# Kernel optimization log

Measured on AMD Instinct MI355X. Metric: run time of the kernel, lower is better.

## Reference

```python
import jax, jax.numpy as jnp
import numpy as np

B, S_IMG, S_TXT, S_BOK = 1, 2048, 512, 4
DM, H, DH, R = 3072, 24, 128, 16
LORA_SCALE, LORA_ALPHA, BOKEH_SCALE = 1.0, 16.0, 1.0
EPS = 1e-6


def _rms_norm(x, w):
    # normalize over head_dim (last axis), Flux RMSNorm eps=1e-6
    var = jnp.mean(jnp.square(x), axis=-1, keepdims=True)
    return x * jax.lax.rsqrt(var + EPS) * w


def _lora(x, w_down, w_up):
    # LoRALinear: up(down(x)) * alpha/rank
    return (x @ w_down.T) @ w_up.T * (LORA_ALPHA / R)


def _apply_rope(x, cos, sin):
    # x: [B,H,S,D]; cos/sin: [S,D]; diffusers use_real=True, unbind_dim=-1 (interleaved pairs)
    x1 = x[..., 0::2]
    x2 = x[..., 1::2]
    rot = jnp.stack([-x2, x1], axis=-1).reshape(x.shape)
    return x * cos[None, None] + rot * sin[None, None]


def _sdpa(q, k, v):
    # q:[B,H,Sq,D] k,v:[B,H,Sk,D]
    scale = 1.0 / jnp.sqrt(jnp.asarray(q.shape[-1], q.dtype))
    scores = jnp.einsum('bhqd,bhkd->bhqk', q, k) * scale
    p = jax.nn.softmax(scores, axis=-1)
    return jnp.einsum('bhqk,bhkd->bhqd', p, v)


def setup_inputs() -> dict:
    key = jax.random.key(0)
    ks = jax.random.split(key, 40)
    std = 0.02
    d = {}
    d['hidden_states'] = jax.random.normal(ks[0], (B, S_IMG, DM), jnp.float32)
    d['encoder_hidden_states'] = jax.random.normal(ks[1], (B, S_TXT, DM), jnp.float32)
    d['bokeh_embeds'] = jax.random.normal(ks[2], (B, S_BOK, DM), jnp.float32)
    theta = jax.random.uniform(ks[3], (S_TXT + S_IMG, DH // 2), jnp.float32) * 2 * np.pi
    theta = jnp.repeat(theta, 2, axis=-1)  # interleaved pairs share angle
    d['rope_cos'] = jnp.cos(theta)
    d['rope_sin'] = jnp.sin(theta)
    # base attention params
    for i, nm in enumerate(['Wq', 'Wk', 'Wv', 'Waq', 'Wak', 'Wav', 'Wo', 'Wao']):
        d[nm] = jax.random.normal(ks[4 + i], (DM, DM), jnp.float32) * std
    for i, nm in enumerate(['bq', 'bk', 'bv', 'baq', 'bak', 'bav', 'bo', 'bao']):
        d[nm] = jax.random.normal(ks[12 + i], (DM,), jnp.float32) * std
    for i, nm in enumerate(['norm_q_w', 'norm_k_w', 'norm_aq_w', 'norm_ak_w']):
        d[nm] = 1.0 + jax.random.normal(ks[20 + i], (DH,), jnp.float32) * std
    # LoRA adapters (up weights random, not zero, for nontrivial math)
    for i, nm in enumerate(['kb_down', 'vb_down', 'qadp_down', 'kadp_down']):
        d[nm] = jax.random.normal(ks[24 + i], (R, DM), jnp.float32) * (1.0 / R)
    for i, nm in enumerate(['kb_up', 'vb_up', 'qadp_up', 'kadp_up']):
        d[nm] = jax.random.normal(ks[28 + i], (DM, R), jnp.float32) * std
    return d


def reference(hidden_states, encoder_hidden_states, bokeh_embeds, rope_cos, rope_sin,
              Wq, Wk, Wv, Waq, Wak, Wav, Wo, Wao,
              bq, bk, bv, baq, bak, bav, bo, bao,
              norm_q_w, norm_k_w, norm_aq_w, norm_ak_w,
              kb_down, vb_down, qadp_down, kadp_down,
              kb_up, vb_up, qadp_up, kadp_up):
    Bsz = encoder_hidden_states.shape[0]

    def heads(x):  # [B,S,DM] -> [B,H,S,DH]
        return x.reshape(Bsz, -1, H, DH).transpose(0, 2, 1, 3)

    q = hidden_states @ Wq.T + bq
    k = hidden_states @ Wk.T + bk
    v = hidden_states @ Wv.T + bv
    q = q + LORA_SCALE * _lora(q, qadp_down, qadp_up)
    k = k + LORA_SCALE * _lora(k, kadp_down, kadp_up)
    q, k, v = heads(q), heads(k), heads(v)
    q = _rms_norm(q, norm_q_w)
    k = _rms_norm(k, norm_k_w)

    eq = heads(encoder_hidden_states @ Waq.T + baq)
    ek = heads(encoder_hidden_states @ Wak.T + bak)
    ev = heads(encoder_hidden_states @ Wav.T + bav)
    eq = _rms_norm(eq, norm_aq_w)
    ek = _rms_norm(ek, norm_ak_w)

    q = jnp.concatenate([eq, q], axis=2)
    k = jnp.concatenate([ek, k], axis=2)
    v = jnp.concatenate([ev, v], axis=2)

    q = _apply_rope(q, rope_cos, rope_sin)
    k = _apply_rope(k, rope_cos, rope_sin)

    out = _sdpa(q, k, v)  # [B,H,S,DH]
    out = out.transpose(0, 2, 1, 3).reshape(Bsz, -1, H * DH)

    # bokeh pass
    kd = heads(_lora(bokeh_embeds, kb_down, kb_up))
    vd = heads(_lora(bokeh_embeds, vb_down, vb_up))
    cam = _sdpa(q, kd, vd).transpose(0, 2, 1, 3).reshape(Bsz, -1, H * DH)
    out = out + BOKEH_SCALE * cam

    enc_out = out[:, :S_TXT]
    img_out = out[:, S_TXT:]
    img_out = img_out @ Wo.T + bo
    enc_out = enc_out @ Wao.T + bao
    return (img_out, enc_out)
```

## Files before the change

### kernel.cpp

```cpp
#include <hip/hip_runtime.h>

#define DMDL 3072
#define SEQ  2560
#define STXT 512
#define HEADS 24
#define DHD  128
#define WB9 9437184

typedef float f32x4 __attribute__((ext_vector_type(4)));
typedef __bf16 bf16x8 __attribute__((ext_vector_type(8)));
typedef unsigned short u16x4 __attribute__((ext_vector_type(4)));

static __device__ __forceinline__ unsigned short f2bf(float f) {
  unsigned u = __float_as_uint(f);
  u += 0x7fffu + ((u >> 16) & 1u);
  return (unsigned short)(u >> 16);
}

static __device__ __forceinline__ float fexp2(float x) {
  return __builtin_amdgcn_exp2f(x);
}

static __device__ __forceinline__ void gload16(const unsigned short* g, unsigned short* l) {
  __builtin_amdgcn_global_load_lds(
      (const __attribute__((address_space(1))) unsigned int*)g,
      (__attribute__((address_space(3))) unsigned int*)l, 16, 0, 0);
}

__global__ __launch_bounds__(256) void convf2b_kernel(
    const float* __restrict__ src, unsigned short* __restrict__ dst) {
  const int idx4 = blockIdx.x * 256 + threadIdx.x;
  float4 v = *(const float4*)(src + (size_t)idx4 * 4);
  u16x4 b = { f2bf(v.x), f2bf(v.y), f2bf(v.z), f2bf(v.w) };
  *(u16x4*)(dst + (size_t)idx4 * 4) = b;
}

__global__ __launch_bounds__(256) void convw_kernel(
    const float* __restrict__ s0, const float* __restrict__ s1,
    const float* __restrict__ s2, unsigned short* __restrict__ dst) {
  const float* src = (blockIdx.y == 0) ? s0 : (blockIdx.y == 1) ? s1 : s2;
  const size_t idx4 = (size_t)blockIdx.x * 256 + threadIdx.x;
  float4 v = *(const float4*)(src + idx4 * 4);
  u16x4 b = { f2bf(v.x), f2bf(v.y), f2bf(v.z), f2bf(v.w) };
  *(u16x4*)(dst + (size_t)blockIdx.y * WB9 + idx4 * 4) = b;
}

__device__ __forceinline__ void gemm_body(
    const unsigned short* __restrict__ A, const unsigned short* __restrict__ Bw,
    const float* __restrict__ bias, float* __restrict__ C,
    int row0, int col0) {
  __shared__ unsigned short Al[128][64];
  __shared__ unsigned short Bl[128][64];
  const int t = threadIdx.x, w = t >> 6, l = t & 63;
  const int wr = (w >> 1) << 6, wc = (w & 1) << 6;
  const int l15 = l & 15, lg = l >> 4;
  f32x4 acc[4][4];
#pragma unroll
  for (int i = 0; i < 4; i++)
#pragma unroll
    for (int j = 0; j < 4; j++) acc[i][j] = (f32x4){0.f, 0.f, 0.f, 0.f};

  for (int k0 = 0; k0 < DMDL; k0 += 64) {
    __syncthreads();
#pragma unroll
    for (int g = 0; g < 4; g++) {
      const int jb = ((w << 2) + g) << 6;
      const int jl = jb + l;
      const int row = jl >> 3, sl = jl & 7;
      const int col = ((sl ^ (row & 7)) << 3);
      gload16(A  + (size_t)(row0 + row) * DMDL + k0 + col, ((unsigned short*)Al) + (size_t)jb * 8);
      gload16(Bw + (size_t)(col0 + row) * DMDL + k0 + col, ((unsigned short*)Bl) + (size_t)jb * 8);
    }
    asm volatile("s_waitcnt vmcnt(0)" ::: "memory");
    __syncthreads();
#pragma unroll
    for (int kf = 0; kf < 2; kf++) {
      bf16x8 af[4], bfr[4];
#pragma unroll
      for (int i = 0; i < 4; i++) {
        const int ra = wr + (i << 4) + l15;
        af[i]  = *(const bf16x8*)&Al[ra][(((kf << 2) + lg) ^ (ra & 7)) << 3];
        const int rb = wc + (i << 4) + l15;
        bfr[i] = *(const bf16x8*)&Bl[rb][(((kf << 2) + lg) ^ (rb & 7)) << 3];
      }
      __builtin_amdgcn_s_setprio(1);
#pragma unroll
      for (int i = 0; i < 4; i++)
#pragma unroll
        for (int j = 0; j < 4; j++)
          acc[i][j] = __builtin_amdgcn_mfma_f32_16x16x32_bf16(af[i], bfr[j], acc[i][j], 0, 0, 0);
      __builtin_amdgcn_s_setprio(0);
    }
  }
#pragma unroll
  for (int i = 0; i < 4; i++)
#pragma unroll
    for (int j = 0; j < 4; j++) {
      const int col = col0 + wc + (j << 4) + l15;
      const float bb = bias[col];
      const int rbase = row0 + wr + (i << 4) + (lg << 2);
#pragma unroll
      for (int r2 = 0; r2 < 4; r2++)
        C[(size_t)(rbase + r2) * DMDL + col] = acc[i][j][r2] + bb;
    }
}

__global__ __launch_bounds__(256) void gemm3_kernel(
    const unsigned short* __restrict__ A, const unsigned short* __restrict__ w3,
    const float* __restrict__ b0, const float* __restrict__ b1, const float* __restrict__ b2,
    float* __restrict__ c0, float* __restrict__ c1, float* __restrict__ c2, int M) {
  const int nwg = (M >> 7) * 72;
  const int cpx = nwg >> 3;
  const int sid = (blockIdx.x & 7) * cpx + (blockIdx.x >> 3);
  const int by = sid / 72, bxx = sid - by * 72;
  const int grp = bxx / 24, bx = bxx - grp * 24;
  const unsigned short* Bw = w3 + (size_t)grp * WB9;
  const float* bias = (grp == 0) ? b0 : (grp == 1) ? b1 : b2;
  float* C = (grp == 0) ? c0 : (grp == 1) ? c1 : c2;
  gemm_body(A, Bw, bias, C, by << 7, bx << 7);
}

__global__ __launch_bounds__(256) void gemm_out_kernel(
    const unsigned short* __restrict__ attnbf, const unsigned short* __restrict__ w3,
    const float* __restrict__ bo, const float* __restrict__ bao,
    float* __restrict__ out) {
  const int sid = (blockIdx.x & 7) * 60 + (blockIdx.x >> 3);
  if (sid < 384) {
    const int by = sid / 24, bx = sid - by * 24;
    gemm_body(attnbf + (size_t)STXT * DMDL, w3, bo, out, by << 7, bx << 7);
  } else {
    const int s2 = sid - 384;
    const int by = s2 / 24, bx = s2 - by * 24;
    gemm_body(attnbf, w3 + WB9, bao, out + (size_t)2048 * DMDL, by << 7, bx << 7);
  }
}

__global__ __launch_bounds__(256) void lora_down2_kernel(
    const float* __restrict__ q0, const float* __restrict__ k0,
    const float* __restrict__ qad, const float* __restrict__ kad,
    float* __restrict__ tmpq, float* __restrict__ tmpk) {
  const int t = threadIdx.x, w = t >> 6, l = t & 63;
  const int m = blockIdx.x;
  const float* X = blockIdx.y ? k0 : q0;
  const float* dwn = blockIdx.y ? kad : qad;
  float* tmp = blockIdx.y ? tmpk : tmpq;
  const float* x = X + (size_t)m * DMDL;
  float acc[16];
#pragma unroll
  for (int r = 0; r < 16; r++) acc[r] = 0.f;
  for (int k = t; k < DMDL; k += 256) {
    float xv = x[k];
#pragma unroll
    for (int r = 0; r < 16; r++) acc[r] += xv * dwn[r * DMDL + k];
  }
#pragma unroll
  for (int off = 1; off < 64; off <<= 1)
#pragma unroll
    for (int r = 0; r < 16; r++) acc[r] += __shfl_xor(acc[r], off);
  __shared__ float red[4][16];
  if (l == 0)
#pragma unroll
    for (int r = 0; r < 16; r++) red[w][r] = acc[r];
  __syncthreads();
  if (t < 16) tmp[(size_t)m * 16 + t] = red[0][t] + red[1][t] + red[2][t] + red[3][t];
}

#define QSCALE 0.12751743f
__global__ __launch_bounds__(256) void pack_kernel(
    const float* __restrict__ q0, const float* __restrict__ k0,
    const float* __restrict__ eq, const float* __restrict__ ek,
    const float* __restrict__ tmpq, const float* __restrict__ tmpk,
    const float* __restrict__ qau, const float* __restrict__ kau,
    const float* __restrict__ nq, const float* __restrict__ nk,
    const float* __restrict__ naq, const float* __restrict__ nak,
    const float* __restrict__ rc, const float* __restrict__ rsn,
    unsigned short* __restrict__ Qp, unsigned short* __restrict__ Kp) {
  const int t = threadIdx.x, w = t >> 6, l = t & 63;
  const int s = blockIdx.x * 4 + w;
  const int h = blockIdx.y;
  const int which = blockIdx.z;
  const int n = h * DHD + 2 * l;
  float2 x;
  const float* nw;
  if (s < STXT) {
    x = *(const float2*)(((which == 0) ? eq : ek) + (size_t)s * DMDL + n);
    nw = (which == 0) ? naq : nak;
  } else {
    x = *(const float2*)(((which == 0) ? q0 : k0) + (size_t)(s - STXT) * DMDL + n);
    nw = (which == 0) ? nq : nk;
    const float* tv = ((which == 0) ? tmpq : tmpk) + (size_t)(s - STXT) * 16;
    const float* uv = ((which == 0) ? qau : kau) + (size_t)n * 16;
    float l1 = 0.f, l2 = 0.f;
#pragma unroll
    for (int r = 0; r < 16; r++) { l1 += tv[r] * uv[r]; l2 += tv[r] * uv[16 + r]; }
    x.x += l1; x.y += l2;
  }
  float ss = x.x * x.x + x.y * x.y;
#pragma unroll
  for (int off = 1; off < 64; off <<= 1) ss += __shfl_xor(ss, off);
  float inv = rsqrtf(ss * (1.f / 128.f) + 1e-6f);
  float xw1 = x.x * inv * nw[2 * l];
  float xw2 = x.y * inv * nw[2 * l + 1];
  float c1 = rc[(size_t)s * DHD + 2 * l], c2 = rc[(size_t)s * DHD + 2 * l + 1];
  float s1 = rsn[(size_t)s * DHD + 2 * l], s2 = rsn[(size_t)s * DHD + 2 * l + 1];
  float y1 = xw1 * c1 - xw2 * s1;
  float y2 = xw2 * c2 + xw1 * s2;
  if (which == 0) { y1 *= QSCALE; y2 *= QSCALE; }
  unsigned short* dst = ((which == 0) ? Qp : Kp) + ((size_t)h * SEQ + s) * DHD + 2 * l;
  unsigned pk = (unsigned)f2bf(y1) | ((unsigned)f2bf(y2) << 16);
  *(unsigned*)dst = pk;
}

__global__ __launch_bounds__(256) void vpackT_kernel(
    const float* __restrict__ v0, const float* __restrict__ ev,
    unsigned short* __restrict__ Vtg) {
  __shared__ unsigned short tile[64][136];
  const int t = threadIdx.x;
  const int s0 = blockIdx.x << 6;
  const int h = blockIdx.y;
  const float* src;
  int srow;
  if (s0 < STXT) { src = ev; srow = s0; } else { src = v0; srow = s0 - STXT; }
#pragma unroll
  for (int p = 0; p < 8; p++) {
    int idx4 = (p << 8) + t;
    int r = idx4 >> 5, c4 = idx4 & 31;
    float4 v = *(const float4*)(src + (size_t)(srow + r) * DMDL + h * DHD + (c4 << 2));
    u16x4 b = { f2bf(v.x), f2bf(v.y), f2bf(v.z), f2bf(v.w) };
    *(u16x4*)&tile[r][c4 << 2] = b;
  }
  __syncthreads();
  const int d = t >> 1, sc = (t & 1) << 5;
  unsigned short outv[32];
#pragma unroll
  for (int e = 0; e < 32; e++) outv[e] = tile[sc + e][d];
  unsigned short* dst = Vtg + ((size_t)h * DHD + d) * SEQ + s0 + sc;
#pragma unroll
  for (int q = 0; q < 4; q++)
    *(uint4*)(dst + (q << 3)) = *(uint4*)&outv[q << 3];
}

__global__ __launch_bounds__(256) void bokeh_down_kernel(
    const float* __restrict__ bok, const float* __restrict__ kbd,
    const float* __restrict__ vbd, float* __restrict__ tkv) {
  const int t = threadIdx.x, w = t >> 6, l = t & 63;
  const int mat = blockIdx.x >> 2, j = blockIdx.x & 3;
  const float* dwn = mat ? vbd : kbd;
  const float* x = bok + (size_t)j * DMDL;
  float acc[16];
#pragma unroll
  for (int r = 0; r < 16; r++) acc[r] = 0.f;
  for (int k = t; k < DMDL; k += 256) {
    float xv = x[k];
#pragma unroll
    for (int r = 0; r < 16; r++) acc[r] += xv * dwn[r * DMDL + k];
  }
#pragma unroll
  for (int off = 1; off < 64; off <<= 1)
#pragma unroll
    for (int r = 0; r < 16; r++) acc[r] += __shfl_xor(acc[r], off);
  __shared__ float red[4][16];
  if (l == 0)
#pragma unroll
    for (int r = 0; r < 16; r++) red[w][r] = acc[r];
  __syncthreads();
  if (t < 16) tkv[(mat * 4 + j) * 16 + t] = red[0][t] + red[1][t] + red[2][t] + red[3][t];
}

__global__ __launch_bounds__(256) void bokeh_up_kernel(
    const float* __restrict__ tkv, const float* __restrict__ kbu,
    const float* __restrict__ vbu, float* __restrict__ kdvd) {
  const int idx = blockIdx.x * 256 + threadIdx.x;
  const int mat = idx / 12288, rem = idx % 12288;
  const int j = rem / DMDL, n = rem % DMDL;
  const float* up = mat ? vbu : kbu;
  const float* tv = tkv + (mat * 4 + j) * 16;
  float s = 0.f;
#pragma unroll
  for (int r = 0; r < 16; r++) s += tv[r] * up[(size_t)n * 16 + r];
  kdvd[(size_t)(mat * 4 + j) * DMDL + n] = s;
}

__global__ __launch_bounds__(256) void attn_kernel(
    const unsigned short* __restrict__ Qp, const unsigned short* __restrict__ Kp,
    const unsigned short* __restrict__ Vtg, const float* __restrict__ kdvd,
    unsigned short* __restrict__ attnbf) {
  __shared__ unsigned short Klds[128][128];
  __shared__ unsigned short Vt[128][128];
  __shared__ unsigned short Plds[4][16][128];
  const int t = threadIdx.x, w = t >> 6, l = t & 63;
  const int l15 = l & 15, lg = l >> 4;
  const int h = blockIdx.y;
  const int q0r = blockIdx.x * 64;
  const unsigned short* Qh = Qp + (size_t)h * SEQ * DHD;
  const unsigned short* Kh = Kp + (size_t)h * SEQ * DHD;
  const unsigned short* Vh = Vtg + (size_t)h * DHD * SEQ;

  bf16x8 qf[4];
  {
    const unsigned short* qsrc = Qh + (size_t)(q0r + w * 16 + l15) * DHD + (lg << 3);
#pragma unroll
    for (int kf = 0; kf < 4; kf++) qf[kf] = *(const bf16x8*)(qsrc + kf * 32);
  }
  f32x4 o[8];
#pragma unroll
  for (int nc = 0; nc < 8; nc++) o[nc] = (f32x4){0.f, 0.f, 0.f, 0.f};
  float m[4] = {-1e30f, -1e30f, -1e30f, -1e30f};
  float sum[4] = {0.f, 0.f, 0.f, 0.f};

  for (int kv0 = 0; kv0 < SEQ; kv0 += 128) {
    __syncthreads();
#pragma unroll
    for (int g = 0; g < 8; g++) {
      const int jb = ((g << 2) + w) << 6;
      const int jl = jb + l;
      const int row = jl >> 4, sl = jl & 15;
      const int col = (sl ^ (row & 7)) << 3;
      gload16(Kh + (size_t)(kv0 + row) * DHD + col, ((unsigned short*)Klds) + (size_t)jb * 8);
      gload16(Vh + (size_t)row * SEQ + kv0 + col, ((unsigned short*)Vt) + (size_t)jb * 8);
    }
    asm volatile("s_waitcnt vmcnt(0)" ::: "memory");
    __syncthreads();
    f32x4 sacc[8];
    __builtin_amdgcn_s_setprio(1);
#pragma unroll
    for (int c = 0; c < 8; c++) {
      sacc[c] = (f32x4){0.f, 0.f, 0.f, 0.f};
      const int krow = c * 16 + l15;
#pragma unroll
      for (int kf = 0; kf < 4; kf++) {
        bf16x8 kb = *(const bf16x8*)&Klds[krow][(((kf << 2) + lg) ^ (krow & 7)) << 3];
        sacc[c] = __builtin_amdgcn_mfma_f32_16x16x32_bf16(qf[kf], kb, sacc[c], 0, 0, 0);
      }
    }
    __builtin_amdgcn_s_setprio(0);
    float mxv[4];
#pragma unroll
    for (int j = 0; j < 4; j++) {
      float mx = sacc[0][j];
#pragma unroll
      for (int c = 1; c < 8; c++) mx = fmaxf(mx, sacc[c][j]);
#pragma unroll
      for (int off = 1; off < 16; off <<= 1) mx = fmaxf(mx, __shfl_xor(mx, off));
      mxv[j] = mx;
    }
    int ok = 1;
#pragma unroll
    for (int j = 0; j < 4; j++) ok &= (mxv[j] <= m[j] + 8.f);
    const bool skip = __all(ok);
    float sc4[4];
#pragma unroll
    for (int j = 0; j < 4; j++) {
      const float mnew = skip ? m[j] : fmaxf(m[j], mxv[j]);
      const int prow = (lg << 2) + j;
      unsigned short* pp = &Plds[w][prow][0];
      float ps = 0.f;
#pragma unroll
      for (int c = 0; c < 8; c++) {
        float pv = fexp2(sacc[c][j] - mnew);
        ps += pv;
        pp[(c * 16 + l15) ^ ((prow & 7) << 3)] = f2bf(pv);
      }
#pragma unroll
      for (int off = 1; off < 16; off <<= 1) ps += __shfl_xor(ps, off);
      if (!skip) {
        float sc = fexp2(m[j] - mnew);
        sum[j] = sum[j] * sc + ps;
        m[j] = mnew;
        sc4[j] = sc;
      } else {
        sum[j] += ps;
      }
    }
    if (!skip) {
#pragma unroll
      for (int nc = 0; nc < 8; nc++) {
        o[nc][0] *= sc4[0]; o[nc][1] *= sc4[1]; o[nc][2] *= sc4[2]; o[nc][3] *= sc4[3];
      }
    }
    __builtin_amdgcn_s_setprio(1);
#pragma unroll
    for (int kf2 = 0; kf2 < 4; kf2++) {
      bf16x8 pa = *(const bf16x8*)&Plds[w][l15][(((kf2 << 2) + lg) ^ (l15 & 7)) << 3];
#pragma unroll
      for (int nc = 0; nc < 8; nc++) {
        const int vrow = nc * 16 + l15;
        bf16x8 vb = *(const bf16x8*)&Vt[vrow][(((kf2 << 2) + lg) ^ (vrow & 7)) << 3];
        o[nc] = __builtin_amdgcn_mfma_f32_16x16x32_bf16(pa, vb, o[nc], 0, 0, 0);
      }
    }
    __builtin_amdgcn_s_setprio(0);
  }

  __syncthreads();
  float* kdl = (float*)&Klds[0][0];
  {
    const int j8 = t >> 5, d4 = (t & 31) << 2;
    *(float4*)&kdl[j8 * 128 + d4] = *(const float4*)(kdvd + (size_t)j8 * DMDL + h * DHD + d4);
  }
  __syncthreads();
  float q32[4][8];
#pragma unroll
  for (int kf = 0; kf < 4; kf++)
#pragma unroll
    for (int r = 0; r < 8; r++) q32[kf][r] = (float)qf[kf][r];
  float pj[4];
#pragma unroll
  for (int jb = 0; jb < 4; jb++) {
    float d = 0.f;
#pragma unroll
    for (int kf = 0; kf < 4; kf++)
#pragma unroll
      for (int r = 0; r < 8; r++)
        d += q32[kf][r] * kdl[jb * 128 + (kf << 5) + (lg << 3) + r];
    d += __shfl_xor(d, 16);
    d += __shfl_xor(d, 32);
    pj[jb] = d;
  }
  float cm = fmaxf(fmaxf(pj[0], pj[1]), fmaxf(pj[2], pj[3]));
  float cs = 0.f;
#pragma unroll
  for (int jb = 0; jb < 4; jb++) { pj[jb] = fexp2(pj[jb] - cm); cs += pj[jb]; }
  float ci = 1.f / cs;
#pragma unroll
  for (int jb = 0; jb < 4; jb++) pj[jb] *= ci;
  float* pnl = kdl + 1024 + (w << 6);
  if (lg == 0) {
#pragma unroll
    for (int jb = 0; jb < 4; jb++) pnl[l15 * 4 + jb] = pj[jb];
  }
  __syncthreads();
  float rinv[4];
#pragma unroll
  for (int j = 0; j < 4; j++) rinv[j] = 1.f / sum[j];
  float pr[4][4];
#pragma unroll
  for (int j = 0; j < 4; j++)
#pragma unroll
    for (int jb = 0; jb < 4; jb++) pr[j][jb] = pnl[(((lg << 2) + j) << 2) + jb];
  const float* vdl = kdl + 512;
#pragma unroll
  for (int nc = 0; nc < 8; nc++) {
    const int col = (nc << 4) + l15;
#pragma unroll
    for (int j = 0; j < 4; j++) {
      float cam = pr[j][0] * vdl[col] + pr[j][1] * vdl[128 + col] +
                  pr[j][2] * vdl[256 + col] + pr[j][3] * vdl[384 + col];
      float outv = o[nc][j] * rinv[j] + cam;
      const int row = q0r + (w << 4) + (lg << 2) + j;
      attnbf[(size_t)row * DMDL + h * DHD + col] = f2bf(outv);
    }
  }
}

extern "C" void kernel_launch(void* const* d_in, const int* in_sizes, int n_in,
                              void* d_out, int out_size, void* d_ws, size_t ws_size,
                              hipStream_t stream) {
  (void)in_sizes; (void)n_in; (void)out_size; (void)ws_size;
  const float* hs  = (const float*)d_in[0];
  const float* enc = (const float*)d_in[1];
  const float* bok = (const float*)d_in[2];
  const float* rc  = (const float*)d_in[3];
  const float* rsn = (const float*)d_in[4];
  const float* Wq  = (const float*)d_in[5];
  const float* Wk  = (const float*)d_in[6];
  const float* Wv  = (const float*)d_in[7];
  const float* Waq = (const float*)d_in[8];
  const float* Wak = (const float*)d_in[9];
  const float* Wav = (const float*)d_in[10];
  const float* Wo  = (const float*)d_in[11];
  const float* Wao = (const float*)d_in[12];
  const float* bq  = (const float*)d_in[13];
  const float* bk  = (const float*)d_in[14];
  const float* bv  = (const float*)d_in[15];
  const float* baq = (const float*)d_in[16];
  const float* bak = (const float*)d_in[17];
  const float* bav = (const float*)d_in[18];
  const float* bo  = (const float*)d_in[19];
  const float* bao = (const float*)d_in[20];
  const float* nq  = (const float*)d_in[21];
  const float* nk  = (const float*)d_in[22];
  const float* naq = (const float*)d_in[23];
  const float* nak = (const float*)d_in[24];
  const float* kbd = (const float*)d_in[25];
  const float* vbd = (const float*)d_in[26];
  const float* qad = (const float*)d_in[27];
  const float* kad = (const float*)d_in[28];
  const float* kbu = (const float*)d_in[29];
  const float* vbu = (const float*)d_in[30];
  const float* qau = (const float*)d_in[31];
  const float* kau = (const float*)d_in[32];

  char* ws = (char*)d_ws;
  unsigned short* w3     = (unsigned short*)(ws + 0);
  unsigned short* hs_bf  = (unsigned short*)(ws + 56623104);
  unsigned short* enc_bf = (unsigned short*)(ws + 69206016);
  float* q0   = (float*)(ws + 72351744);
  float* k0   = (float*)(ws + 97517568);
  float* v0   = (float*)(ws + 122683392);
  float* eq   = (float*)(ws + 147849216);
  float* ek   = (float*)(ws + 154140672);
  float* ev   = (float*)(ws + 160432128);
  float* tmpq = (float*)(ws + 166723584);
  float* tmpk = (float*)(ws + 166854656);
  float* tkv  = (float*)(ws + 166985728);
  float* kdvd = (float*)(ws + 166986240);
  unsigned short* Qp  = (unsigned short*)(ws + 167084544);
  unsigned short* Kp  = (unsigned short*)(ws + 182813184);
  unsigned short* Vtg = (unsigned short*)(ws + 72351744);
  unsigned short* attnbf = (unsigned short*)(ws + 122683392);

  float* out = (float*)d_out;

  dim3 blk(256);

  convf2b_kernel<<<6144, blk, 0, stream>>>(hs, hs_bf);
  convf2b_kernel<<<1536, blk, 0, stream>>>(enc, enc_bf);
  bokeh_down_kernel<<<8, blk, 0, stream>>>(bok, kbd, vbd, tkv);
  bokeh_up_kernel<<<96, blk, 0, stream>>>(tkv, kbu, vbu, kdvd);

  convw_kernel<<<dim3(9216, 3), blk, 0, stream>>>(Wq, Wk, Wv, w3);
  gemm3_kernel<<<1152, blk, 0, stream>>>(hs_bf, w3, bq, bk, bv, q0, k0, v0, 2048);
  convw_kernel<<<dim3(9216, 3), blk, 0, stream>>>(Waq, Wak, Wav, w3);
  gemm3_kernel<<<288, blk, 0, stream>>>(enc_bf, w3, baq, bak, bav, eq, ek, ev, 512);

  lora_down2_kernel<<<dim3(2048, 2), blk, 0, stream>>>(q0, k0, qad, kad, tmpq, tmpk);

  pack_kernel<<<dim3(SEQ / 4, HEADS, 2), blk, 0, stream>>>(
      q0, k0, eq, ek, tmpq, tmpk, qau, kau, nq, nk, naq, nak, rc, rsn, Qp, Kp);
  vpackT_kernel<<<dim3(SEQ / 64, HEADS), blk, 0, stream>>>(v0, ev, Vtg);

  attn_kernel<<<dim3(SEQ / 64, HEADS), blk, 0, stream>>>(Qp, Kp, Vtg, kdvd, attnbf);

  convw_kernel<<<dim3(9216, 2), blk, 0, stream>>>(Wo, Wao, Wao, w3);
  gemm_out_kernel<<<480, blk, 0, stream>>>(attnbf, w3, bo, bao, out);
}
```

Baseline: 740.2 us.

## Double-buffer LDS in bf16 GEMMs and enlarge tile to 128x256 with 512 threads

Rewrites the shared GEMM core to use two LDS buffers, so the global-to-LDS loads for the next K tile overlap the MFMA work on the current tile. The output tile grows from 128x128 to 128x256 and the block from 256 to 512 threads (8 waves in a 2x4 layout). Grid sizes and the XCD-aware block remapping in the QKV and output GEMM launches are adjusted to match. The larger tile improves reuse of the A operand but uses more LDS (96KB) and launches half as many blocks, which may reduce occupancy and wave-level parallelism.

```diff
diff --git a/kernel.cpp b/kernel.cpp
--- a/kernel.cpp
+++ b/kernel.cpp
@@ -45,14 +45,14 @@
   *(u16x4*)(dst + (size_t)blockIdx.y * WB9 + idx4 * 4) = b;
 }
 
-__device__ __forceinline__ void gemm_body(
+__device__ __forceinline__ void gemm_core(
     const unsigned short* __restrict__ A, const unsigned short* __restrict__ Bw,
     const float* __restrict__ bias, float* __restrict__ C,
     int row0, int col0) {
-  __shared__ unsigned short Al[128][64];
-  __shared__ unsigned short Bl[128][64];
+  __shared__ unsigned short sA[2][128][64];
+  __shared__ unsigned short sB[2][256][64];
   const int t = threadIdx.x, w = t >> 6, l = t & 63;
-  const int wr = (w >> 1) << 6, wc = (w & 1) << 6;
+  const int wm = w >> 2, wn = w & 3;
   const int l15 = l & 15, lg = l >> 4;
   f32x4 acc[4][4];
 #pragma unroll
@@ -60,78 +60,106 @@
 #pragma unroll
     for (int j = 0; j < 4; j++) acc[i][j] = (f32x4){0.f, 0.f, 0.f, 0.f};
 
-  for (int k0 = 0; k0 < DMDL; k0 += 64) {
-    __syncthreads();
-#pragma unroll
-    for (int g = 0; g < 4; g++) {
-      const int jb = ((w << 2) + g) << 6;
-      const int jl = jb + l;
-      const int row = jl >> 3, sl = jl & 7;
-      const int col = ((sl ^ (row & 7)) << 3);
-      gload16(A  + (size_t)(row0 + row) * DMDL + k0 + col, ((unsigned short*)Al) + (size_t)jb * 8);
-      gload16(Bw + (size_t)(col0 + row) * DMDL + k0 + col, ((unsigned short*)Bl) + (size_t)jb * 8);
-    }
+#define STAGE_TILE(kt, buf)                                                     \
+  {                                                                             \
+    const int kk = (kt) << 6;                                                   \
+    _Pragma("unroll")                                                           \
+    for (int g = 0; g < 2; g++) {                                               \
+      const int jb = (g << 3) + w;                                              \
+      const int u = (jb << 6) + l;                                              \
+      const int row = u >> 3, sl = u & 7;                                       \
+      const int col = (sl ^ (row & 7)) << 3;                                    \
+      gload16(A + (size_t)(row0 + row) * DMDL + kk + col,                       \
+              &sA[buf][0][0] + (size_t)(jb << 9));                              \
+    }                                                                           \
+    _Pragma("unroll")                                                           \
+    for (int g = 0; g < 4; g++) {                                               \
+      const int jb = (g << 3) + w;                                              \
+      const int u = (jb << 6) + l;                                              \
+      const int row = u >> 3, sl = u & 7;                                       \
+      const int col = (sl ^ (row & 7)) << 3;                                    \
+      gload16(Bw + (size_t)(col0 + row) * DMDL + kk + col,                      \
+              &sB[buf][0][0] + (size_t)(jb << 9));                              \
+    }                                                                           \
+  }
+
+  STAGE_TILE(0, 0)
+  asm volatile("s_waitcnt vmcnt(0)" ::: "memory");
+  __syncthreads();
+
+  const int NT = DMDL / 64;
+  for (int kt = 0; kt < NT; kt++) {
+    const int cur = kt & 1;
+    if (kt + 1 < NT) STAGE_TILE(kt + 1, cur ^ 1)
+    bf16x8 bfr[2][4], af[2][4];
+#pragma unroll
+    for (int kf = 0; kf < 2; kf++)
+#pragma unroll
+      for (int j = 0; j < 4; j++) {
+        const int rb = (wn << 6) + (j << 4) + l15;
+        bfr[kf][j] = *(const bf16x8*)&sB[cur][rb][(((kf << 2) + lg) ^ (rb & 7)) << 3];
+      }
+#pragma unroll
+    for (int kf = 0; kf < 2; kf++)
+#pragma unroll
+      for (int i = 0; i < 4; i++) {
+        const int ra = (wm << 6) + (i << 4) + l15;
+        af[kf][i] = *(const bf16x8*)&sA[cur][ra][(((kf << 2) + lg) ^ (ra & 7)) << 3];
+      }
+    __builtin_amdgcn_s_setprio(1);
+#pragma unroll
+    for (int kf = 0; kf < 2; kf++)
+#pragma unroll
+      for (int i = 0; i < 4; i++)
+#pragma unroll
+        for (int j = 0; j < 4; j++)
+          acc[i][j] = __builtin_amdgcn_mfma_f32_16x16x32_bf16(af[kf][i], bfr[kf][j], acc[i][j], 0, 0, 0);
+    __builtin_amdgcn_s_setprio(0);
     asm volatile("s_waitcnt vmcnt(0)" ::: "memory");
     __syncthreads();
-#pragma unroll
-    for (int kf = 0; kf < 2; kf++) {
-      bf16x8 af[4], bfr[4];
-#pragma unroll
-      for (int i = 0; i < 4; i++) {
-        const int ra = wr + (i << 4) + l15;
-        af[i]  = *(const bf16x8*)&Al[ra][(((kf << 2) + lg) ^ (ra & 7)) << 3];
-        const int rb = wc + (i << 4) + l15;
-        bfr[i] = *(const bf16x8*)&Bl[rb][(((kf << 2) + lg) ^ (rb & 7)) << 3];
-      }
-      __builtin_amdgcn_s_setprio(1);
-#pragma unroll
-      for (int i = 0; i < 4; i++)
-#pragma unroll
-        for (int j = 0; j < 4; j++)
-          acc[i][j] = __builtin_amdgcn_mfma_f32_16x16x32_bf16(af[i], bfr[j], acc[i][j], 0, 0, 0);
-      __builtin_amdgcn_s_setprio(0);
-    }
-  }
+  }
+#undef STAGE_TILE
+
 #pragma unroll
   for (int i = 0; i < 4; i++)
 #pragma unroll
     for (int j = 0; j < 4; j++) {
-      const int col = col0 + wc + (j << 4) + l15;
+      const int col = col0 + (wn << 6) + (j << 4) + l15;
       const float bb = bias[col];
-      const int rbase = row0 + wr + (i << 4) + (lg << 2);
+      const int rbase = row0 + (wm << 6) + (i << 4) + (lg << 2);
 #pragma unroll
       for (int r2 = 0; r2 < 4; r2++)
         C[(size_t)(rbase + r2) * DMDL + col] = acc[i][j][r2] + bb;
     }
 }
 
-__global__ __launch_bounds__(256) void gemm3_kernel(
+__global__ __launch_bounds__(512) void gemm3_kernel(
     const unsigned short* __restrict__ A, const unsigned short* __restrict__ w3,
     const float* __restrict__ b0, const float* __restrict__ b1, const float* __restrict__ b2,
     float* __restrict__ c0, float* __restrict__ c1, float* __restrict__ c2, int M) {
-  const int nwg = (M >> 7) * 72;
+  const int nwg = (M >> 7) * 36;
   const int cpx = nwg >> 3;
   const int sid = (blockIdx.x & 7) * cpx + (blockIdx.x >> 3);
-  const int by = sid / 72, bxx = sid - by * 72;
-  const int grp = bxx / 24, bx = bxx - grp * 24;
+  const int by = sid / 36, bxx = sid - by * 36;
+  const int grp = bxx / 12, bx = bxx - grp * 12;
   const unsigned short* Bw = w3 + (size_t)grp * WB9;
   const float* bias = (grp == 0) ? b0 : (grp == 1) ? b1 : b2;
   float* C = (grp == 0) ? c0 : (grp == 1) ? c1 : c2;
-  gemm_body(A, Bw, bias, C, by << 7, bx << 7);
-}
-
-__global__ __launch_bounds__(256) void gemm_out_kernel(
+  gemm_core(A, Bw, bias, C, by << 7, bx << 8);
+}
+
+__global__ __launch_bounds__(512) void gemm_out_kernel(
     const unsigned short* __restrict__ attnbf, const unsigned short* __restrict__ w3,
     const float* __restrict__ bo, const float* __restrict__ bao,
     float* __restrict__ out) {
-  const int sid = (blockIdx.x & 7) * 60 + (blockIdx.x >> 3);
-  if (sid < 384) {
-    const int by = sid / 24, bx = sid - by * 24;
-    gemm_body(attnbf + (size_t)STXT * DMDL, w3, bo, out, by << 7, bx << 7);
+  const int sid = (blockIdx.x & 7) * 30 + (blockIdx.x >> 3);
+  if (sid < 192) {
+    const int by = sid / 12, bx = sid - by * 12;
+    gemm_core(attnbf + (size_t)STXT * DMDL, w3, bo, out, by << 7, bx << 8);
   } else {
-    const int s2 = sid - 384;
-    const int by = s2 / 24, bx = s2 - by * 24;
-    gemm_body(attnbf, w3 + WB9, bao, out + (size_t)2048 * DMDL, by << 7, bx << 7);
+    const int s2 = sid - 192;
+    const int by = s2 / 12, bx = s2 - by * 12;
+    gemm_core(attnbf, w3 + WB9, bao, out + (size_t)2048 * DMDL, by << 7, bx << 8);
   }
 }
 
@@ -513,6 +541,7 @@
   float* out = (float*)d_out;
 
   dim3 blk(256);
+  dim3 blk512(512);
 
   convf2b_kernel<<<6144, blk, 0, stream>>>(hs, hs_bf);
   convf2b_kernel<<<1536, blk, 0, stream>>>(enc, enc_bf);
@@ -520,9 +549,9 @@
   bokeh_up_kernel<<<96, blk, 0, stream>>>(tkv, kbu, vbu, kdvd);
 
   convw_kernel<<<dim3(9216, 3), blk, 0, stream>>>(Wq, Wk, Wv, w3);
-  gemm3_kernel<<<1152, blk, 0, stream>>>(hs_bf, w3, bq, bk, bv, q0, k0, v0, 2048);
+  gemm3_kernel<<<576, blk512, 0, stream>>>(hs_bf, w3, bq, bk, bv, q0, k0, v0, 2048);
   convw_kernel<<<dim3(9216, 3), blk, 0, stream>>>(Waq, Wak, Wav, w3);
-  gemm3_kernel<<<288, blk, 0, stream>>>(enc_bf, w3, baq, bak, bav, eq, ek, ev, 512);
+  gemm3_kernel<<<144, blk512, 0, stream>>>(enc_bf, w3, baq, bak, bav, eq, ek, ev, 512);
 
   lora_down2_kernel<<<dim3(2048, 2), blk, 0, stream>>>(q0, k0, qad, kad, tmpq, tmpk);
 
@@ -533,5 +562,5 @@
   attn_kernel<<<dim3(SEQ / 64, HEADS), blk, 0, stream>>>(Qp, Kp, Vtg, kdvd, attnbf);
 
   convw_kernel<<<dim3(9216, 2), blk, 0, stream>>>(Wo, Wao, Wao, w3);
-  gemm_out_kernel<<<480, blk, 0, stream>>>(attnbf, w3, bo, bao, out);
-}
+  gemm_out_kernel<<<240, blk512, 0, stream>>>(attnbf, w3, bo, bao, out);
+}
```

Result: slower. 792.9 us (+7.1%).
